# Kernel tuning notes

Measured on AMD Instinct MI355X. Metric: run time of the kernel, lower is better.

## Reference

```python
import jax, jax.numpy as jnp
import numpy as np

B, S, D = 1, 2048, 4096
H, KVH, HD = 32, 8, 128
WIN = 2048
REPEATS = H // KVH
SCALE = HD ** -0.5
NEG = -1e9


def setup_inputs() -> dict:
    key = jax.random.key(0)
    ks = jax.random.split(key, 5)
    x = jax.random.normal(ks[0], (B, S, D), dtype=jnp.float32) * 0.02
    wq = jax.random.normal(ks[1], (H * HD, D), dtype=jnp.float32) * (D ** -0.5)
    wk = jax.random.normal(ks[2], (KVH * HD, D), dtype=jnp.float32) * (D ** -0.5)
    wv = jax.random.normal(ks[3], (KVH * HD, D), dtype=jnp.float32) * (D ** -0.5)
    wo = jax.random.normal(ks[4], (H * HD, D), dtype=jnp.float32).T * ((H * HD) ** -0.5)
    wo = jnp.asarray(wo)  # [D, H*HD] torch-style (out, in) = (D, H*HD)
    positions = jnp.arange(S, dtype=jnp.int32)
    # rotary tables: freqs_cis[s, j] = exp(i * s * theta_j), theta_j = 10000^(-2j/HD)
    theta = 10000.0 ** (-jnp.arange(0, HD, 2, dtype=jnp.float32) / HD)  # [HD/2]
    ang = positions[:, None].astype(jnp.float32) * theta[None, :]       # [S, HD/2]
    freqs_cos = jnp.cos(ang)
    freqs_sin = jnp.sin(ang)
    # sliding-window causal additive mask [S, S]
    i = jnp.arange(S)[:, None]
    j = jnp.arange(S)[None, :]
    allowed = (j <= i) & (i - j < WIN)
    mask = jnp.where(allowed, 0.0, NEG).astype(jnp.float32)
    return {"x": x, "freqs_cos": freqs_cos, "freqs_sin": freqs_sin,
            "wq": wq, "wk": wk, "wv": wv, "wo": wo,
            "mask": mask, "positions": positions}


def _apply_rope(t, cos, sin):
    # t: [B, S, h, HD]; pairs are (even, odd) interleaved -> complex mul
    tr = t[..., 0::2]  # real parts [B,S,h,HD/2]
    ti = t[..., 1::2]  # imag parts
    c = cos[None, :, None, :]
    s = sin[None, :, None, :]
    out_r = tr * c - ti * s
    out_i = tr * s + ti * c
    return jnp.stack([out_r, out_i], axis=-1).reshape(t.shape)


def reference(x, freqs_cos, freqs_sin, wq, wk, wv, wo, mask, positions):
    bsz, seqlen, _ = x.shape
    q = (x @ wq.T).reshape(bsz, seqlen, H, HD)
    k = (x @ wk.T).reshape(bsz, seqlen, KVH, HD)
    v = (x @ wv.T).reshape(bsz, seqlen, KVH, HD)
    q = _apply_rope(q, freqs_cos, freqs_sin)
    k = _apply_rope(k, freqs_cos, freqs_sin)
    # GQA: repeat_interleave kv heads to match query heads (prefill path)
    k = jnp.repeat(k, REPEATS, axis=2)  # [B,S,H,HD]
    v = jnp.repeat(v, REPEATS, axis=2)
    scores = jnp.einsum("bqhd,bkhd->bhqk", q, k) * SCALE
    scores = scores + mask[None, None, :, :]
    probs = jax.nn.softmax(scores, axis=-1)
    out = jnp.einsum("bhqk,bkhd->bqhd", probs, v)
    out = out.reshape(bsz, seqlen, H * HD)
    return out @ wo.T
```

## Files before the change

### kernel.cpp

```cpp
#include <hip/hip_runtime.h>
#include <hip/hip_bf16.h>
#include <stdint.h>

#define SEQ    2048
#define DMODEL 4096
#define NH     32
#define NKVH   8
#define HDIM   128
#define KVD    (NKVH*HDIM)
#define QD     (NH*HDIM)
#define QKVN   (QD + 2*KVD)
#define ASCALE 0.08838834764831845f

typedef __attribute__((ext_vector_type(8))) short s8v;
typedef __attribute__((ext_vector_type(4))) short s4v;
typedef __attribute__((ext_vector_type(4))) float f4v;

#define MFMA16(acc, a, b) \
  asm("v_mfma_f32_16x16x32_bf16 %0, %1, %2, %0" : "+v"(acc) : "v"(a), "v"(b))

#define SBAR() do { __builtin_amdgcn_sched_barrier(0); \
                    __builtin_amdgcn_s_barrier();      \
                    __builtin_amdgcn_sched_barrier(0); } while (0)

__device__ __forceinline__ void gl2lds16(const void* g, void* l) {
  __builtin_amdgcn_global_load_lds(
      (const __attribute__((address_space(1))) void*)g,
      (__attribute__((address_space(3))) void*)l, 16, 0, 0);
}

__device__ __forceinline__ void store_out(__hip_bfloat16* p, float v) { *p = __float2bfloat16(v); }
__device__ __forceinline__ void store_out(float* p, float v) { *p = v; }

__global__ __launch_bounds__(256) void k_cvt(const float* __restrict__ in,
                                             __hip_bfloat16* __restrict__ out, int n8,
                                             float scale) {
  int i = blockIdx.x * 256 + threadIdx.x;
  if (i >= n8) return;
  const float4* p = (const float4*)in + (size_t)i * 2;
  float4 a = p[0], b = p[1];
  union { __hip_bfloat16 h[8]; s8v v; } o;
  o.h[0] = __float2bfloat16(a.x * scale); o.h[1] = __float2bfloat16(a.y * scale);
  o.h[2] = __float2bfloat16(a.z * scale); o.h[3] = __float2bfloat16(a.w * scale);
  o.h[4] = __float2bfloat16(b.x * scale); o.h[5] = __float2bfloat16(b.y * scale);
  o.h[6] = __float2bfloat16(b.z * scale); o.h[7] = __float2bfloat16(b.w * scale);
  *(s8v*)(out + (size_t)i * 8) = o.v;
}

__global__ __launch_bounds__(256) void k_rope(__hip_bfloat16* __restrict__ t,
                                              const float* __restrict__ fc,
                                              const float* __restrict__ fs, int heads) {
  int pid = blockIdx.x * 256 + threadIdx.x;
  int i = pid & 63;
  int rest = pid >> 6;
  int h = rest % heads;
  int s = rest / heads;
  size_t base = ((size_t)s * heads + h) * HDIM + 2 * i;
  uint32_t u = *(const uint32_t*)(t + base);
  __hip_bfloat16 hh[2]; *(uint32_t*)hh = u;
  float tr = __bfloat162float(hh[0]), ti = __bfloat162float(hh[1]);
  float c = fc[(size_t)s * 64 + i], sv = fs[(size_t)s * 64 + i];
  hh[0] = __float2bfloat16(tr * c - ti * sv);
  hh[1] = __float2bfloat16(tr * sv + ti * c);
  *(uint32_t*)(t + base) = *(uint32_t*)hh;
}

__global__ __launch_bounds__(512, 2) void k_qkv(const __hip_bfloat16* __restrict__ A,
                                                const __hip_bfloat16* __restrict__ W,
                                                __hip_bfloat16* __restrict__ Qb,
                                                __hip_bfloat16* __restrict__ Kc,
                                                __hip_bfloat16* __restrict__ Vt) {
  __shared__ __align__(16) __hip_bfloat16 sm[2][256 * 64 + 192 * 64];
  const int t5 = threadIdx.x;
  const int wave = t5 >> 6, lane = t5 & 63;
  const int lrow = lane & 15, kq = lane >> 4;
  const int wm = wave >> 2, wn = wave & 3;
  const int mt = blockIdx.x & 7, nt = blockIdx.x >> 3;
  const int m0 = mt * 256, n0 = nt * 192;

  auto stageA = [&](int p, int kt) {
#pragma unroll
    for (int it = 0; it < 4; ++it) {
      int chunk = it * 512 + t5;
      int r = chunk >> 3, cc = ((chunk & 7) ^ (r & 7)) * 8;
      gl2lds16(A + (size_t)(m0 + r) * DMODEL + kt * 64 + cc,
               (char*)&sm[p][0] + it * 8192 + wave * 1024);
    }
  };
  auto stageB = [&](int p, int kt) {
#pragma unroll
    for (int it = 0; it < 3; ++it) {
      int chunk = it * 512 + t5;
      int r = chunk >> 3, cc = ((chunk & 7) ^ (r & 7)) * 8;
      gl2lds16(W + (size_t)(n0 + r) * DMODEL + kt * 64 + cc,
               (char*)&sm[p][0] + 32768 + it * 8192 + wave * 1024);
    }
  };

  f4v acc[8][3] = {};

  stageA(0, 0); stageB(0, 0);
  stageA(1, 1); stageB(1, 1);

  const int NT = DMODEL / 64;
#pragma unroll 2
  for (int t = 0; t < NT; ++t) {
    const int p = t & 1;
    const __hip_bfloat16* As = &sm[p][0];
    const __hip_bfloat16* Bs = &sm[p][256 * 64];

    __builtin_amdgcn_sched_barrier(0);
    if (t == NT - 1) asm volatile("s_waitcnt vmcnt(0)" ::: "memory");
    else             asm volatile("s_waitcnt vmcnt(7)" ::: "memory");
    __builtin_amdgcn_s_barrier();
    __builtin_amdgcn_sched_barrier(0);

    s8v a0[8], b0[3];
#pragma unroll
    for (int m = 0; m < 8; ++m) {
      int row = wm * 128 + m * 16 + lrow;
      a0[m] = *(const s8v*)&As[row * 64 + ((kq * 8) ^ ((row & 7) << 3))];
    }
#pragma unroll
    for (int n = 0; n < 3; ++n) {
      int row = wn * 48 + n * 16 + lrow;
      b0[n] = *(const s8v*)&Bs[row * 64 + ((kq * 8) ^ ((row & 7) << 3))];
    }
    __builtin_amdgcn_s_setprio(1);
#pragma unroll
    for (int m = 0; m < 4; ++m)
#pragma unroll
      for (int n = 0; n < 3; ++n) MFMA16(acc[m][n], a0[m], b0[n]);
    __builtin_amdgcn_s_setprio(0);
    SBAR();

    s8v a1[8], b1[3];
#pragma unroll
    for (int m = 0; m < 8; ++m) {
      int row = wm * 128 + m * 16 + lrow;
      a1[m] = *(const s8v*)&As[row * 64 + ((32 + kq * 8) ^ ((row & 7) << 3))];
    }
#pragma unroll
    for (int n = 0; n < 3; ++n) {
      int row = wn * 48 + n * 16 + lrow;
      b1[n] = *(const s8v*)&Bs[row * 64 + ((32 + kq * 8) ^ ((row & 7) << 3))];
    }
    __builtin_amdgcn_s_setprio(1);
#pragma unroll
    for (int m = 4; m < 8; ++m)
#pragma unroll
      for (int n = 0; n < 3; ++n) MFMA16(acc[m][n], a0[m], b0[n]);
    __builtin_amdgcn_s_setprio(0);
    SBAR();

    if (t + 2 < NT) stageA(p, t + 2);
    __builtin_amdgcn_s_setprio(1);
#pragma unroll
    for (int m = 0; m < 4; ++m)
#pragma unroll
      for (int n = 0; n < 3; ++n) MFMA16(acc[m][n], a1[m], b1[n]);
    __builtin_amdgcn_s_setprio(0);
    SBAR();

    if (t + 2 < NT) stageB(p, t + 2);
    __builtin_amdgcn_s_setprio(1);
#pragma unroll
    for (int m = 4; m < 8; ++m)
#pragma unroll
      for (int n = 0; n < 3; ++n) MFMA16(acc[m][n], a1[m], b1[n]);
    __builtin_amdgcn_s_setprio(0);
  }

#pragma unroll
  for (int m = 0; m < 8; ++m)
#pragma unroll
    for (int n = 0; n < 3; ++n) {
      int c = n0 + wn * 48 + n * 16 + lrow;
      int r0 = m0 + wm * 128 + m * 16 + kq * 4;
      if (c < QD) {
#pragma unroll
        for (int j = 0; j < 4; ++j)
          Qb[(size_t)(r0 + j) * QD + c] = __float2bfloat16(acc[m][n][j]);
      } else if (c < QD + KVD) {
#pragma unroll
        for (int j = 0; j < 4; ++j)
          Kc[(size_t)(r0 + j) * KVD + (c - QD)] = __float2bfloat16(acc[m][n][j]);
      } else {
        union { __hip_bfloat16 b[4]; s4v v; } u;
#pragma unroll
        for (int j = 0; j < 4; ++j) u.b[j] = __float2bfloat16(acc[m][n][j]);
        *(s4v*)&Vt[(size_t)(c - QD - KVD) * SEQ + r0] = u.v;
      }
    }
}

template <typename OT>
__global__ __launch_bounds__(256) void k_gemm_bt(const __hip_bfloat16* __restrict__ A,
                                                 const __hip_bfloat16* __restrict__ B,
                                                 OT* __restrict__ C, int M, int N, int K) {
  __shared__ __align__(16) __hip_bfloat16 As[128 * 64];
  __shared__ __align__(16) __hip_bfloat16 Bs[128 * 64];
  const int t = threadIdx.x;
  const int wave = t >> 6, lane = t & 63;
  const int lrow = lane & 15, kq = lane >> 4;
  const int wr = wave >> 1, wc = wave & 1;
  const int m0 = blockIdx.y * 128, n0 = blockIdx.x * 128;

  f4v acc[4][4] = {};

  for (int k0 = 0; k0 < K; k0 += 64) {
#pragma unroll
    for (int it = 0; it < 4; ++it) {
      int chunk = it * 256 + t;
      int r = chunk >> 3;
      int cc = ((chunk & 7) ^ (r & 7)) * 8;
      gl2lds16(A + (size_t)(m0 + r) * K + k0 + cc, (char*)As + it * 4096 + wave * 1024);
      gl2lds16(B + (size_t)(n0 + r) * K + k0 + cc, (char*)Bs + it * 4096 + wave * 1024);
    }
    __syncthreads();
#pragma unroll
    for (int kk = 0; kk < 64; kk += 32) {
      s8v af[4], bfr[4];
#pragma unroll
      for (int m = 0; m < 4; ++m) {
        int row = wr * 64 + m * 16 + lrow;
        af[m] = *(const s8v*)&As[row * 64 + ((kk + kq * 8) ^ ((row & 7) << 3))];
      }
#pragma unroll
      for (int n = 0; n < 4; ++n) {
        int row = wc * 64 + n * 16 + lrow;
        bfr[n] = *(const s8v*)&Bs[row * 64 + ((kk + kq * 8) ^ ((row & 7) << 3))];
      }
#pragma unroll
      for (int m = 0; m < 4; ++m)
#pragma unroll
        for (int n = 0; n < 4; ++n)
          MFMA16(acc[m][n], af[m], bfr[n]);
    }
    __syncthreads();
  }

#pragma unroll
  for (int m = 0; m < 4; ++m)
#pragma unroll
    for (int n = 0; n < 4; ++n)
#pragma unroll
      for (int j = 0; j < 4; ++j) {
        int r = m0 + wr * 64 + m * 16 + kq * 4 + j;
        int c = n0 + wc * 64 + n * 16 + lrow;
        store_out(&C[(size_t)r * N + c], acc[m][n][j]);
      }
}

__global__ __launch_bounds__(256, 2) void k_flash(const __hip_bfloat16* __restrict__ Q,
                                                  const __hip_bfloat16* __restrict__ Kb,
                                                  const __hip_bfloat16* __restrict__ Vtg,
                                                  __hip_bfloat16* __restrict__ O) {
  __shared__ __align__(16) __hip_bfloat16 Ks[2][64 * 128];
  __shared__ __align__(16) __hip_bfloat16 Vs[144 * 64];
  __shared__ __align__(16) __hip_bfloat16 Ps[4][16 * 64];
  const int qp = blockIdx.x, h = blockIdx.y, g = h >> 2;
  const int t = threadIdx.x, wave = t >> 6, lane = t & 63;
  const int lrow = lane & 15, kq = lane >> 4;
  const int qtA = qp, qtB = 31 - qp;

  s8v qfA[4], qfB[4];
  {
    const int qrA = qtA * 64 + wave * 16 + lrow;
    const int qrB = qtB * 64 + wave * 16 + lrow;
#pragma unroll
    for (int tt = 0; tt < 4; ++tt) {
      qfA[tt] = *(const s8v*)(Q + (size_t)qrA * QD + h * HDIM + tt * 32 + kq * 8);
      qfB[tt] = *(const s8v*)(Q + (size_t)qrB * QD + h * HDIM + tt * 32 + kq * 8);
    }
  }

  if (t < 128) {
    union { __hip_bfloat16 h8[8]; s8v v; } one;
#pragma unroll
    for (int e = 0; e < 8; ++e) one.h8[e] = __float2bfloat16(1.0f);
    *(s8v*)&Vs[128 * 64 + t * 8] = one.v;
  }

  f4v oA[9] = {}, oB[9] = {};
  float mA[4], mB[4];
#pragma unroll
  for (int j = 0; j < 4; ++j) { mA[j] = mB[j] = -1e30f; }

  auto stage_k = [&](int buf, int kv) {
#pragma unroll
    for (int it = 0; it < 4; ++it) {
      int chunk = it * 256 + t;
      int r = chunk >> 4, cc = ((chunk & 15) ^ (r & 7)) * 8;
      gl2lds16(Kb + (size_t)(kv * 64 + r) * KVD + g * HDIM + cc,
               (char*)&Ks[buf][0] + it * 4096 + wave * 1024);
    }
  };
  auto stage_v = [&](int kv) {
#pragma unroll
    for (int it = 0; it < 4; ++it) {
      int chunk = it * 256 + t;
      int d = chunk >> 3, cc = ((chunk & 7) ^ (d & 7)) * 8;
      gl2lds16(Vtg + (size_t)(g * HDIM + d) * SEQ + kv * 64 + cc,
               (char*)Vs + it * 4096 + wave * 1024);
    }
  };

  auto soft_pv = [&](f4v (&s)[4], int qt, int kv, f4v (&acc_o)[9], float (&mrun)[4]) {
    __hip_bfloat16* P = &Ps[wave][0];
    const bool diag = (kv == qt);
    asm volatile("" ::: "memory");
#pragma unroll
    for (int j = 0; j < 4; ++j) {
      float p4[4];
      float mx = -1e30f;
#pragma unroll
      for (int n = 0; n < 4; ++n) {
        float v = s[n][j];
        if (diag) {
          const int qi = qt * 64 + wave * 16 + kq * 4 + j;
          int ki = kv * 64 + n * 16 + lrow;
          if (ki > qi) v = -1e30f;
        }
        p4[n] = v;
        mx = fmaxf(mx, v);
      }
#pragma unroll
      for (int msk = 1; msk < 16; msk <<= 1) mx = fmaxf(mx, __shfl_xor(mx, msk, 64));
      if (!__all(mx <= mrun[j])) {
        float mnew = fmaxf(mrun[j], mx);
        float fsc = __expf(mrun[j] - mnew);
        mrun[j] = mnew;
#pragma unroll
        for (int n = 0; n < 9; ++n) acc_o[n][j] *= fsc;
      }
      const int drow = kq * 4 + j;
#pragma unroll
      for (int n = 0; n < 4; ++n) {
        float p = __expf(p4[n] - mrun[j]);
        P[drow * 64 + ((n * 16 + lrow) ^ ((drow & 7) << 3))] = __float2bfloat16(p);
      }
    }
    asm volatile("" ::: "memory");
#pragma unroll
    for (int tt = 0; tt < 2; ++tt) {
      s8v pa = *(const s8v*)&P[lrow * 64 + ((tt * 32 + kq * 8) ^ ((lrow & 7) << 3))];
#pragma unroll
      for (int n = 0; n < 9; ++n) {
        int d = n * 16 + lrow;
        s8v vf = *(const s8v*)&Vs[d * 64 + ((tt * 32 + kq * 8) ^ ((d & 7) << 3))];
        MFMA16(acc_o[n], pa, vf);
      }
    }
  };

  stage_k(0, 0);
  int cur = 0;
  for (int kv = 0; kv <= qtB; ++kv) {
    const bool actA = (kv <= qtA);
    __syncthreads();
    if (kv < qtB) stage_k(cur ^ 1, kv + 1);
    stage_v(kv);

    f4v sB[4] = {}, sA[4] = {};
    if (actA) {
#pragma unroll
      for (int tt = 0; tt < 4; ++tt)
#pragma unroll
        for (int n = 0; n < 4; ++n) {
          int row = n * 16 + lrow;
          s8v kf = *(const s8v*)&Ks[cur][row * 128 + ((tt * 32 + kq * 8) ^ ((row & 7) << 3))];
          MFMA16(sB[n], qfB[tt], kf);
          MFMA16(sA[n], qfA[tt], kf);
        }
    } else {
#pragma unroll
      for (int tt = 0; tt < 4; ++tt)
#pragma unroll
        for (int n = 0; n < 4; ++n) {
          int row = n * 16 + lrow;
          s8v kf = *(const s8v*)&Ks[cur][row * 128 + ((tt * 32 + kq * 8) ^ ((row & 7) << 3))];
          MFMA16(sB[n], qfB[tt], kf);
        }
    }
    __syncthreads();

    soft_pv(sB, qtB, kv, oB, mB);
    if (actA) soft_pv(sA, qtA, kv, oA, mA);
    cur ^= 1;
  }

#pragma unroll
  for (int n = 0; n < 8; ++n)
#pragma unroll
    for (int j = 0; j < 4; ++j) {
      int d = n * 16 + lrow;
      int qiB = qtB * 64 + wave * 16 + kq * 4 + j;
      O[(size_t)qiB * QD + h * HDIM + d] = __float2bfloat16(oB[n][j] / oB[8][j]);
      int qiA = qtA * 64 + wave * 16 + kq * 4 + j;
      O[(size_t)qiA * QD + h * HDIM + d] = __float2bfloat16(oA[n][j] / oA[8][j]);
    }
}

extern "C" void kernel_launch(void* const* d_in, const int* in_sizes, int n_in,
                              void* d_out, int out_size, void* d_ws, size_t ws_size,
                              hipStream_t stream) {
  const float* x  = (const float*)d_in[0];
  const float* fc = (const float*)d_in[1];
  const float* fs = (const float*)d_in[2];
  const float* wq = (const float*)d_in[3];
  const float* wk = (const float*)d_in[4];
  const float* wv = (const float*)d_in[5];
  const float* wo = (const float*)d_in[6];
  float* out = (float*)d_out;

  char* ws = (char*)d_ws;
  auto alloc = [&](size_t bytes) {
    char* p = ws;
    ws += (bytes + 255) & ~(size_t)255;
    return p;
  };
  __hip_bfloat16* xb  = (__hip_bfloat16*)alloc((size_t)SEQ * DMODEL * 2);
  __hip_bfloat16* wf  = (__hip_bfloat16*)alloc((size_t)QKVN * DMODEL * 2);
  __hip_bfloat16* wob = (__hip_bfloat16*)alloc((size_t)DMODEL * QD * 2);
  __hip_bfloat16* Qb  = (__hip_bfloat16*)alloc((size_t)SEQ * QD * 2);
  __hip_bfloat16* Kc  = (__hip_bfloat16*)alloc((size_t)SEQ * KVD * 2);
  __hip_bfloat16* Vtg = (__hip_bfloat16*)alloc((size_t)KVD * SEQ * 2);
  __hip_bfloat16* Ob  = (__hip_bfloat16*)alloc((size_t)SEQ * QD * 2);

  auto cvt = [&](const float* src, __hip_bfloat16* dst, size_t n, float scale) {
    int n8 = (int)(n / 8);
    k_cvt<<<dim3((n8 + 255) / 256), dim3(256), 0, stream>>>(src, dst, n8, scale);
  };
  cvt(x,  xb, (size_t)SEQ * DMODEL, 1.0f);
  cvt(wq, wf, (size_t)QD * DMODEL, ASCALE);
  cvt(wk, wf + (size_t)QD * DMODEL, (size_t)KVD * DMODEL, 1.0f);
  cvt(wv, wf + (size_t)(QD + KVD) * DMODEL, (size_t)KVD * DMODEL, 1.0f);
  cvt(wo, wob, (size_t)DMODEL * QD, 1.0f);

  k_qkv<<<dim3(256), dim3(512), 0, stream>>>(xb, wf, Qb, Kc, Vtg);

  k_rope<<<dim3(SEQ * NH * 64 / 256), 256, 0, stream>>>(Qb, fc, fs, NH);
  k_rope<<<dim3(SEQ * NKVH * 64 / 256), 256, 0, stream>>>(Kc, fc, fs, NKVH);

  k_flash<<<dim3(16, NH), 256, 0, stream>>>(Qb, Kc, Vtg, Ob);

  k_gemm_bt<float><<<dim3(DMODEL / 128, SEQ / 128), 256, 0, stream>>>(Ob, wob, out, SEQ, DMODEL, DMODEL);
}
```

Before: 300.1 us.

## Replace output projection GEMM with double-buffered 128x256 tile kernel

The generic single-buffered 128x128 output-projection GEMM becomes a specialised kernel. It uses 512 threads, 128x256 tiles and double-buffered LDS, issuing the next tile's async global-to-LDS loads while the MFMAs run. It interleaves fragment reads with MFMA groups under sched barriers and setprio, and waits with explicit vmcnt. The aim is to hide global load latency and cut barrier stalls, at the cost of more LDS per block and a grid of only 256 blocks.

Measured after the change: 294.9 us. Within noise of the previous version (-1.8%).

```diff
diff --git a/kernel.cpp b/kernel.cpp
--- a/kernel.cpp
+++ b/kernel.cpp
@@ -28,9 +28,6 @@
       (const __attribute__((address_space(1))) void*)g,
       (__attribute__((address_space(3))) void*)l, 16, 0, 0);
 }
-
-__device__ __forceinline__ void store_out(__hip_bfloat16* p, float v) { *p = __float2bfloat16(v); }
-__device__ __forceinline__ void store_out(float* p, float v) { *p = v; }
 
 __global__ __launch_bounds__(256) void k_cvt(const float* __restrict__ in,
                                              __hip_bfloat16* __restrict__ out, int n8,
@@ -194,50 +191,107 @@
     }
 }
 
-template <typename OT>
-__global__ __launch_bounds__(256) void k_gemm_bt(const __hip_bfloat16* __restrict__ A,
-                                                 const __hip_bfloat16* __restrict__ B,
-                                                 OT* __restrict__ C, int M, int N, int K) {
-  __shared__ __align__(16) __hip_bfloat16 As[128 * 64];
-  __shared__ __align__(16) __hip_bfloat16 Bs[128 * 64];
-  const int t = threadIdx.x;
-  const int wave = t >> 6, lane = t & 63;
+__global__ __launch_bounds__(512, 2) void k_oproj(const __hip_bfloat16* __restrict__ A,
+                                                  const __hip_bfloat16* __restrict__ B,
+                                                  float* __restrict__ C) {
+  __shared__ __align__(16) __hip_bfloat16 sm[2][128 * 64 + 256 * 64];
+  const int t5 = threadIdx.x;
+  const int wave = t5 >> 6, lane = t5 & 63;
   const int lrow = lane & 15, kq = lane >> 4;
-  const int wr = wave >> 1, wc = wave & 1;
-  const int m0 = blockIdx.y * 128, n0 = blockIdx.x * 128;
+  const int wm = wave >> 2, wn = wave & 3;
+  const int m0 = blockIdx.y * 128, n0 = blockIdx.x * 256;
+
+  auto stageA = [&](int p, int kt) {
+#pragma unroll
+    for (int it = 0; it < 2; ++it) {
+      int chunk = it * 512 + t5;
+      int r = chunk >> 3, cc = ((chunk & 7) ^ (r & 7)) * 8;
+      gl2lds16(A + (size_t)(m0 + r) * QD + kt * 64 + cc,
+               (char*)&sm[p][0] + it * 8192 + wave * 1024);
+    }
+  };
+  auto stageB = [&](int p, int kt) {
+#pragma unroll
+    for (int it = 0; it < 4; ++it) {
+      int chunk = it * 512 + t5;
+      int r = chunk >> 3, cc = ((chunk & 7) ^ (r & 7)) * 8;
+      gl2lds16(B + (size_t)(n0 + r) * QD + kt * 64 + cc,
+               (char*)&sm[p][0] + 16384 + it * 8192 + wave * 1024);
+    }
+  };
 
   f4v acc[4][4] = {};
 
-  for (int k0 = 0; k0 < K; k0 += 64) {
-#pragma unroll
-    for (int it = 0; it < 4; ++it) {
-      int chunk = it * 256 + t;
-      int r = chunk >> 3;
-      int cc = ((chunk & 7) ^ (r & 7)) * 8;
-      gl2lds16(A + (size_t)(m0 + r) * K + k0 + cc, (char*)As + it * 4096 + wave * 1024);
-      gl2lds16(B + (size_t)(n0 + r) * K + k0 + cc, (char*)Bs + it * 4096 + wave * 1024);
-    }
-    __syncthreads();
-#pragma unroll
-    for (int kk = 0; kk < 64; kk += 32) {
-      s8v af[4], bfr[4];
-#pragma unroll
-      for (int m = 0; m < 4; ++m) {
-        int row = wr * 64 + m * 16 + lrow;
-        af[m] = *(const s8v*)&As[row * 64 + ((kk + kq * 8) ^ ((row & 7) << 3))];
-      }
-#pragma unroll
-      for (int n = 0; n < 4; ++n) {
-        int row = wc * 64 + n * 16 + lrow;
-        bfr[n] = *(const s8v*)&Bs[row * 64 + ((kk + kq * 8) ^ ((row & 7) << 3))];
-      }
-#pragma unroll
-      for (int m = 0; m < 4; ++m)
-#pragma unroll
-        for (int n = 0; n < 4; ++n)
-          MFMA16(acc[m][n], af[m], bfr[n]);
-    }
-    __syncthreads();
+  stageA(0, 0); stageB(0, 0);
+  stageA(1, 1); stageB(1, 1);
+
+  const int NT = QD / 64;
+#pragma unroll 2
+  for (int t = 0; t < NT; ++t) {
+    const int p = t & 1;
+    const __hip_bfloat16* As = &sm[p][0];
+    const __hip_bfloat16* Bs = &sm[p][128 * 64];
+
+    __builtin_amdgcn_sched_barrier(0);
+    if (t == NT - 1) asm volatile("s_waitcnt vmcnt(0)" ::: "memory");
+    else             asm volatile("s_waitcnt vmcnt(6)" ::: "memory");
+    __builtin_amdgcn_s_barrier();
+    __builtin_amdgcn_sched_barrier(0);
+
+    s8v a0[4], b0[4];
+#pragma unroll
+    for (int m = 0; m < 4; ++m) {
+      int row = wm * 64 + m * 16 + lrow;
+      a0[m] = *(const s8v*)&As[row * 64 + ((kq * 8) ^ ((row & 7) << 3))];
+    }
+#pragma unroll
+    for (int n = 0; n < 4; ++n) {
+      int row = wn * 64 + n * 16 + lrow;
+      b0[n] = *(const s8v*)&Bs[row * 64 + ((kq * 8) ^ ((row & 7) << 3))];
+    }
+    __builtin_amdgcn_s_setprio(1);
+#pragma unroll
+    for (int m = 0; m < 2; ++m)
+#pragma unroll
+      for (int n = 0; n < 4; ++n) MFMA16(acc[m][n], a0[m], b0[n]);
+    __builtin_amdgcn_s_setprio(0);
+    SBAR();
+
+    s8v a1[4], b1[4];
+#pragma unroll
+    for (int m = 0; m < 4; ++m) {
+      int row = wm * 64 + m * 16 + lrow;
+      a1[m] = *(const s8v*)&As[row * 64 + ((32 + kq * 8) ^ ((row & 7) << 3))];
+    }
+#pragma unroll
+    for (int n = 0; n < 4; ++n) {
+      int row = wn * 64 + n * 16 + lrow;
+      b1[n] = *(const s8v*)&Bs[row * 64 + ((32 + kq * 8) ^ ((row & 7) << 3))];
+    }
+    __builtin_amdgcn_s_setprio(1);
+#pragma unroll
+    for (int m = 2; m < 4; ++m)
+#pragma unroll
+      for (int n = 0; n < 4; ++n) MFMA16(acc[m][n], a0[m], b0[n]);
+    __builtin_amdgcn_s_setprio(0);
+    SBAR();
+
+    if (t + 2 < NT) stageA(p, t + 2);
+    __builtin_amdgcn_s_setprio(1);
+#pragma unroll
+    for (int m = 0; m < 2; ++m)
+#pragma unroll
+      for (int n = 0; n < 4; ++n) MFMA16(acc[m][n], a1[m], b1[n]);
+    __builtin_amdgcn_s_setprio(0);
+    SBAR();
+
+    if (t + 2 < NT) stageB(p, t + 2);
+    __builtin_amdgcn_s_setprio(1);
+#pragma unroll
+    for (int m = 2; m < 4; ++m)
+#pragma unroll
+      for (int n = 0; n < 4; ++n) MFMA16(acc[m][n], a1[m], b1[n]);
+    __builtin_amdgcn_s_setprio(0);
   }
 
 #pragma unroll
@@ -246,9 +300,9 @@
     for (int n = 0; n < 4; ++n)
 #pragma unroll
       for (int j = 0; j < 4; ++j) {
-        int r = m0 + wr * 64 + m * 16 + kq * 4 + j;
-        int c = n0 + wc * 64 + n * 16 + lrow;
-        store_out(&C[(size_t)r * N + c], acc[m][n][j]);
+        int r = m0 + wm * 64 + m * 16 + kq * 4 + j;
+        int c = n0 + wn * 64 + n * 16 + lrow;
+        C[(size_t)r * DMODEL + c] = acc[m][n][j];
       }
 }
 
@@ -445,5 +499,5 @@
 
   k_flash<<<dim3(16, NH), 256, 0, stream>>>(Qb, Kc, Vtg, Ob);
 
-  k_gemm_bt<float><<<dim3(DMODEL / 128, SEQ / 128), 256, 0, stream>>>(Ob, wob, out, SEQ, DMODEL, DMODEL);
-}
+  k_oproj<<<dim3(DMODEL / 256, SEQ / 128), dim3(512), 0, stream>>>(Ob, wob, out);
+}
```
